# Kernel tuning notes

Measured on AMD Instinct MI355X. Metric: run time of the kernel, lower is better.

## Reference

```python
import jax, jax.numpy as jnp
import numpy as np

DIM = 1024
HEADS = 16
B, N = 4, 1024

def setup_inputs() -> dict:
    key = jax.random.key(0)
    k1, k2, k3 = jax.random.split(key, 3)
    x = jax.random.normal(k1, (B, N, DIM), dtype=jnp.float32)
    # xavier-uniform-ish init scale
    Wqkv = jax.random.normal(k2, (3 * DIM, DIM), dtype=jnp.float32) * (1.0 / np.sqrt(DIM))
    bqkv = jnp.zeros((3 * DIM,), dtype=jnp.float32)
    W1 = jax.random.normal(k3, (DIM, DIM), dtype=jnp.float32) * (1.0 / np.sqrt(DIM))
    b1 = jnp.zeros((DIM,), dtype=jnp.float32)
    return {"x": x, "Wqkv": Wqkv, "bqkv": bqkv, "W1": W1, "b1": b1}

def reference(x, Wqkv, bqkv, W1, b1):
    b, n, dim = x.shape
    h = HEADS
    d = dim // h
    scale = dim ** (-0.5)  # NOTE: module scales by full dim, not head dim
    qkv = x @ Wqkv.T + bqkv  # [b, n, 3*dim]
    qkv = qkv.reshape(b, n, 3, h, d)
    q = jnp.transpose(qkv[:, :, 0], (0, 2, 1, 3))  # [b, h, n, d]
    k = jnp.transpose(qkv[:, :, 1], (0, 2, 1, 3))
    v = jnp.transpose(qkv[:, :, 2], (0, 2, 1, 3))
    dots = jnp.einsum('bhid,bhjd->bhij', q, k) * scale
    attn = jax.nn.softmax(dots, axis=-1)
    out = jnp.einsum('bhij,bhjd->bhid', attn, v)
    out = jnp.transpose(out, (0, 2, 1, 3)).reshape(b, n, dim)
    out = out @ W1.T + b1
    return out
```

## Files before the change

kernel.cpp:

```cpp
#include <hip/hip_runtime.h>
#include <cmath>

typedef __bf16 bf16;
typedef __bf16 bf16x8 __attribute__((ext_vector_type(8)));
typedef __bf16 bf16x4 __attribute__((ext_vector_type(4)));
typedef float f32x4 __attribute__((ext_vector_type(4)));

#define MFMA16(a, b, c) __builtin_amdgcn_mfma_f32_16x16x32_bf16(a, b, c, 0, 0, 0)

__device__ __forceinline__ void load_lds16(const void* g, void* l) {
    __builtin_amdgcn_global_load_lds(
        (const __attribute__((address_space(1))) void*)g,
        (__attribute__((address_space(3))) void*)l, 16, 0, 0);
}

__device__ __forceinline__ bf16x8 load8(const bf16* p) { return *(const bf16x8*)p; }
__device__ __forceinline__ bf16x8 load8(const float* p) {
    float4 f0 = *(const float4*)p;
    float4 f1 = *(const float4*)(p + 4);
    bf16x8 r;
    r[0] = (bf16)f0.x; r[1] = (bf16)f0.y; r[2] = (bf16)f0.z; r[3] = (bf16)f0.w;
    r[4] = (bf16)f1.x; r[5] = (bf16)f1.y; r[6] = (bf16)f1.z; r[7] = (bf16)f1.w;
    return r;
}

__global__ __launch_bounds__(256) void cvt3(
    const float* __restrict__ s0, bf16* __restrict__ d0, int n0,
    const float* __restrict__ s1, bf16* __restrict__ d1, int n1,
    const float* __restrict__ s2, bf16* __restrict__ d2, int n2)
{
    int i = blockIdx.x * 256 + threadIdx.x;
    const float* s; bf16* d; int base;
    if (i < n0)                { s = s0; d = d0; base = i; }
    else if (i < n0 + n1)      { s = s1; d = d1; base = i - n0; }
    else if (i < n0 + n1 + n2) { s = s2; d = d2; base = i - n0 - n1; }
    else return;
    *(bf16x8*)(d + (size_t)base * 8) = load8(s + (size_t)base * 8);
}

template <int EPI, typename TB, int BN>
__global__ __launch_bounds__(256) void gemm_bt(
    const bf16* __restrict__ A, const TB* __restrict__ Bm,
    const float* __restrict__ bias,
    bf16* __restrict__ qo, bf16* __restrict__ ko, bf16* __restrict__ vto,
    float* __restrict__ C, int M, int N, int K)
{
    constexpr int WN = BN / 2;
    constexpr int JN = WN / 16;
    constexpr int SLOTS = (128 + BN) * 8;

    __shared__ bf16 As[128 * 64];
    __shared__ bf16 Bs[BN * 64];

    const int tid = threadIdx.x;
    const int l   = tid & 63;
    const int w   = tid >> 6;
    const int wm  = w & 1, wn = w >> 1;
    const int l15 = l & 15;
    const int g   = l >> 4;
    const int swz = l15 & 7;
    const int m0  = blockIdx.y * 128;
    const int n0  = blockIdx.x * BN;

    f32x4 acc[4][JN] = {};

    for (int k0 = 0; k0 < K; k0 += 64) {
        __syncthreads();
        #pragma unroll
        for (int it = 0; it < SLOTS / 256; ++it) {
            int s = it * 256 + w * 64 + l;
            if (s < 1024) {
                int row = s >> 3, pc = s & 7;
                int lc  = pc ^ (row & 7);
                load_lds16(A + (size_t)(m0 + row) * K + k0 + lc * 8, &As[s * 8]);
            } else {
                int t = s - 1024;
                int row = t >> 3, pc = t & 7;
                int lc  = pc ^ (row & 7);
                if constexpr (sizeof(TB) == 2) {
                    load_lds16(Bm + (size_t)(n0 + row) * K + k0 + lc * 8, &Bs[t * 8]);
                } else {
                    *(bf16x8*)&Bs[t * 8] = load8(Bm + (size_t)(n0 + row) * K + k0 + lc * 8);
                }
            }
        }
        __syncthreads();
        #pragma unroll
        for (int kk = 0; kk < 64; kk += 32) {
            bf16x8 aF[4], bF[JN];
            #pragma unroll
            for (int i = 0; i < 4; ++i)
                aF[i] = *(const bf16x8*)&As[(wm * 64 + i * 16 + l15) * 64
                                            + ((((kk >> 3) + g) ^ swz) * 8)];
            #pragma unroll
            for (int j = 0; j < JN; ++j)
                bF[j] = *(const bf16x8*)&Bs[(wn * WN + j * 16 + l15) * 64
                                            + ((((kk >> 3) + g) ^ swz) * 8)];
            #pragma unroll
            for (int i = 0; i < 4; ++i)
                #pragma unroll
                for (int j = 0; j < JN; ++j)
                    acc[i][j] = MFMA16(aF[i], bF[j], acc[i][j]);
        }
    }

    #pragma unroll
    for (int j = 0; j < JN; ++j) {
        int gcol = n0 + wn * WN + j * 16 + l15;
        float bv = bias[gcol];
        if (EPI == 0) {
            int which = gcol >> 10;
            int h  = (gcol >> 6) & 15;
            int dd = gcol & 63;
            #pragma unroll
            for (int i = 0; i < 4; ++i) {
                #pragma unroll
                for (int r = 0; r < 4; ++r) {
                    int grow = m0 + wm * 64 + i * 16 + g * 4 + r;
                    int b    = grow >> 10;
                    int npos = grow & 1023;
                    float v  = acc[i][j][r] + bv;
                    size_t bh = (size_t)(b * 16 + h);
                    if (which == 0)
                        qo[(bh * 1024 + npos) * 64 + dd] = (bf16)v;
                    else if (which == 1)
                        ko[(bh * 1024 + npos) * 64 + dd] = (bf16)v;
                    else
                        vto[(bh * 64 + dd) * 1024 + npos] = (bf16)v;
                }
            }
        } else {
            #pragma unroll
            for (int i = 0; i < 4; ++i)
                #pragma unroll
                for (int r = 0; r < 4; ++r) {
                    int grow = m0 + wm * 64 + i * 16 + g * 4 + r;
                    C[(size_t)grow * N + gcol] = acc[i][j][r] + bv;
                }
        }
    }
}

__global__ __launch_bounds__(256) void attn_fused(
    const bf16* __restrict__ qb, const bf16* __restrict__ kb,
    const bf16* __restrict__ vtb, bf16* __restrict__ attn)
{
    __shared__ bf16 Ks[64 * 64];
    __shared__ bf16 Vts[64 * 64];
    __shared__ bf16 Ps[4][32][72];

    const int tid = threadIdx.x;
    const int l   = tid & 63;
    const int w   = tid >> 6;
    const int l15 = l & 15;
    const int g   = l >> 4;
    const int swz = l15 & 7;
    const int bid = blockIdx.x;
    const int bh  = bid & 63;
    const int qc  = bid >> 6;
    const int m0  = qc * 128 + w * 32;

    const bf16* q_bh  = qb  + (size_t)bh * 65536;
    const bf16* k_bh  = kb  + (size_t)bh * 65536;
    const bf16* vt_bh = vtb + (size_t)bh * 65536;

    bf16x8 qf[2][2];
    #pragma unroll
    for (int mi = 0; mi < 2; ++mi)
        #pragma unroll
        for (int kk = 0; kk < 2; ++kk)
            qf[mi][kk] = *(const bf16x8*)(q_bh
                + (size_t)(m0 + mi * 16 + l15) * 64 + kk * 32 + g * 8);

    f32x4 o[2][4] = {};
    float lsum[2] = {0.f, 0.f};
    const float C_EXP = 0.04508422f;

    for (int jt = 0; jt < 16; ++jt) {
        const int j0 = jt * 64;
        __syncthreads();
        #pragma unroll
        for (int it = 0; it < 2; ++it) {
            int s   = it * 256 + tid;
            int row = s >> 3, pc = s & 7;
            int lc  = pc ^ (row & 7);
            load_lds16(k_bh + (size_t)(j0 + row) * 64 + lc * 8, &Ks[s * 8]);
            load_lds16(vt_bh + (size_t)row * 1024 + j0 + lc * 8, &Vts[s * 8]);
        }
        __syncthreads();

        bf16x8 kf[2][4], vf[2][4];
        #pragma unroll
        for (int kk = 0; kk < 2; ++kk)
            #pragma unroll
            for (int js = 0; js < 4; ++js) {
                int off = (js * 16 + l15) * 64 + (((kk * 4 + g) ^ swz) * 8);
                kf[kk][js] = *(const bf16x8*)&Ks[off];
                vf[kk][js] = *(const bf16x8*)&Vts[off];
            }

        #pragma unroll
        for (int mi = 0; mi < 2; ++mi) {
            f32x4 s4[4] = {};
            #pragma unroll
            for (int kk = 0; kk < 2; ++kk)
                #pragma unroll
                for (int js = 0; js < 4; ++js)
                    s4[js] = MFMA16(kf[kk][js], qf[mi][kk], s4[js]);
            float ls = 0.f;
            #pragma unroll
            for (int js = 0; js < 4; ++js) {
                bf16x4 pk;
                #pragma unroll
                for (int r = 0; r < 4; ++r) {
                    pk[r] = (bf16)exp2f(s4[js][r] * C_EXP);
                    ls += (float)pk[r];
                }
                *(bf16x4*)&Ps[w][mi * 16 + l15][js * 16 + g * 4] = pk;
            }
            lsum[mi] += ls;
        }
        __syncthreads();

        #pragma unroll
        for (int kk = 0; kk < 2; ++kk) {
            bf16x8 pf[2];
            #pragma unroll
            for (int mi = 0; mi < 2; ++mi)
                pf[mi] = *(const bf16x8*)&Ps[w][mi * 16 + l15][kk * 32 + g * 8];
            #pragma unroll
            for (int mi = 0; mi < 2; ++mi)
                #pragma unroll
                for (int ns = 0; ns < 4; ++ns)
                    o[mi][ns] = MFMA16(pf[mi], vf[kk][ns], o[mi][ns]);
        }
    }

    #pragma unroll
    for (int mi = 0; mi < 2; ++mi) {
        float t = lsum[mi];
        t += __shfl_xor(t, 16);
        t += __shfl_xor(t, 32);
        #pragma unroll
        for (int r = 0; r < 4; ++r) {
            float inv = 1.0f / __shfl(t, g * 4 + r);
            int grow = m0 + mi * 16 + g * 4 + r;
            size_t obase = ((size_t)(bh >> 4) * 1024 + grow) * 1024 + (bh & 15) * 64;
            #pragma unroll
            for (int ns = 0; ns < 4; ++ns)
                attn[obase + ns * 16 + l15] = (bf16)(o[mi][ns][r] * inv);
        }
    }
}

extern "C" void kernel_launch(void* const* d_in, const int* in_sizes, int n_in,
                              void* d_out, int out_size, void* d_ws, size_t ws_size,
                              hipStream_t stream)
{
    const float* x    = (const float*)d_in[0];
    const float* Wqkv = (const float*)d_in[1];
    const float* bqkv = (const float*)d_in[2];
    const float* W1   = (const float*)d_in[3];
    const float* b1   = (const float*)d_in[4];
    float* out = (float*)d_out;

    const size_t SEG = (size_t)4 * 16 * 1024 * 64;
    bf16* xbf  = (bf16*)d_ws;
    bf16* qb   = xbf + SEG;
    bf16* kb   = qb + SEG;
    bf16* vtb  = kb + SEG;
    bf16* attnb = xbf;
    bf16* wqkvbf = vtb + SEG;
    bf16* w1bf   = wqkvbf + 3145728;

    const bool cw = ws_size >= (size_t)(5 * SEG) * sizeof(bf16);

    const int nx = 524288;
    const int nw = cw ? 393216 : 0;
    const int n1 = cw ? 131072 : 0;
    const int tot = nx + nw + n1;
    cvt3<<<dim3((tot + 255) / 256), 256, 0, stream>>>(
        x, xbf, nx, Wqkv, wqkvbf, nw, W1, w1bf, n1);

    if (cw)
        gemm_bt<0, bf16, 128><<<dim3(24, 32), 256, 0, stream>>>(
            xbf, wqkvbf, bqkv, qb, kb, vtb, nullptr, 4096, 3072, 1024);
    else
        gemm_bt<0, float, 128><<<dim3(24, 32), 256, 0, stream>>>(
            xbf, Wqkv, bqkv, qb, kb, vtb, nullptr, 4096, 3072, 1024);

    attn_fused<<<dim3(512), 256, 0, stream>>>(qb, kb, vtb, attnb);

    if (cw)
        gemm_bt<1, bf16, 64><<<dim3(16, 32), 256, 0, stream>>>(
            attnb, w1bf, b1, nullptr, nullptr, nullptr, out, 4096, 1024, 1024);
    else
        gemm_bt<1, float, 64><<<dim3(16, 32), 256, 0, stream>>>(
            attnb, W1, b1, nullptr, nullptr, nullptr, out, 4096, 1024, 1024);
}
```

Before: 174.3 us.

## Halve attention query tile per block, double blocks, and load 128-key tiles

```diff
diff --git a/kernel.cpp b/kernel.cpp
--- a/kernel.cpp
+++ b/kernel.cpp
@@ -141,13 +141,13 @@
     }
 }
 
-__global__ __launch_bounds__(256) void attn_fused(
+__global__ __launch_bounds__(256, 4) void attn_fused(
     const bf16* __restrict__ qb, const bf16* __restrict__ kb,
     const bf16* __restrict__ vtb, bf16* __restrict__ attn)
 {
-    __shared__ bf16 Ks[64 * 64];
-    __shared__ bf16 Vts[64 * 64];
-    __shared__ bf16 Ps[4][32][72];
+    __shared__ __align__(16) bf16 Ks[2 * 64 * 64];
+    __shared__ __align__(16) bf16 Vts[2 * 64 * 64];
+    __shared__ __align__(16) bf16 Ps[4 * 16 * 64];
 
     const int tid = threadIdx.x;
     const int l   = tid & 63;
@@ -158,55 +158,58 @@
     const int bid = blockIdx.x;
     const int bh  = bid & 63;
     const int qc  = bid >> 6;
-    const int m0  = qc * 128 + w * 32;
+    const int m0  = qc * 64 + w * 16;
 
     const bf16* q_bh  = qb  + (size_t)bh * 65536;
     const bf16* k_bh  = kb  + (size_t)bh * 65536;
     const bf16* vt_bh = vtb + (size_t)bh * 65536;
 
-    bf16x8 qf[2][2];
+    bf16x8 qf[2];
     #pragma unroll
-    for (int mi = 0; mi < 2; ++mi)
-        #pragma unroll
-        for (int kk = 0; kk < 2; ++kk)
-            qf[mi][kk] = *(const bf16x8*)(q_bh
-                + (size_t)(m0 + mi * 16 + l15) * 64 + kk * 32 + g * 8);
-
-    f32x4 o[2][4] = {};
-    float lsum[2] = {0.f, 0.f};
+    for (int kk = 0; kk < 2; ++kk)
+        qf[kk] = *(const bf16x8*)(q_bh + (size_t)(m0 + l15) * 64 + kk * 32 + g * 8);
+
+    f32x4 o[4] = {};
+    float lsum = 0.f;
     const float C_EXP = 0.04508422f;
 
-    for (int jt = 0; jt < 16; ++jt) {
-        const int j0 = jt * 64;
-        __syncthreads();
-        #pragma unroll
-        for (int it = 0; it < 2; ++it) {
-            int s   = it * 256 + tid;
-            int row = s >> 3, pc = s & 7;
-            int lc  = pc ^ (row & 7);
-            load_lds16(k_bh + (size_t)(j0 + row) * 64 + lc * 8, &Ks[s * 8]);
-            load_lds16(vt_bh + (size_t)row * 1024 + j0 + lc * 8, &Vts[s * 8]);
-        }
-        __syncthreads();
-
-        bf16x8 kf[2][4], vf[2][4];
-        #pragma unroll
-        for (int kk = 0; kk < 2; ++kk)
-            #pragma unroll
-            for (int js = 0; js < 4; ++js) {
-                int off = (js * 16 + l15) * 64 + (((kk * 4 + g) ^ swz) * 8);
-                kf[kk][js] = *(const bf16x8*)&Ks[off];
-                vf[kk][js] = *(const bf16x8*)&Vts[off];
-            }
-
-        #pragma unroll
-        for (int mi = 0; mi < 2; ++mi) {
+    for (int jt = 0; jt < 8; ++jt) {
+        const int j0 = jt * 128;
+        __syncthreads();
+        #pragma unroll
+        for (int h = 0; h < 2; ++h)
+            #pragma unroll
+            for (int it = 0; it < 2; ++it) {
+                int s   = it * 256 + tid;
+                int row = s >> 3;
+                int lc  = (s & 7) ^ (row & 7);
+                load_lds16(k_bh + (size_t)(j0 + h * 64 + row) * 64 + lc * 8,
+                           &Ks[h * 4096 + s * 8]);
+                load_lds16(vt_bh + (size_t)row * 1024 + j0 + h * 64 + lc * 8,
+                           &Vts[h * 4096 + s * 8]);
+            }
+        __syncthreads();
+
+        #pragma unroll
+        for (int h = 0; h < 2; ++h) {
+            bf16x8 kf[2][4], vf[2][4];
+            #pragma unroll
+            for (int kk = 0; kk < 2; ++kk)
+                #pragma unroll
+                for (int js = 0; js < 4; ++js) {
+                    int off = h * 4096 + (js * 16 + l15) * 64
+                            + (((kk * 4 + g) ^ swz) * 8);
+                    kf[kk][js] = *(const bf16x8*)&Ks[off];
+                    vf[kk][js] = *(const bf16x8*)&Vts[off];
+                }
+
             f32x4 s4[4] = {};
             #pragma unroll
             for (int kk = 0; kk < 2; ++kk)
                 #pragma unroll
                 for (int js = 0; js < 4; ++js)
-                    s4[js] = MFMA16(kf[kk][js], qf[mi][kk], s4[js]);
+                    s4[js] = MFMA16(kf[kk][js], qf[kk], s4[js]);
+
             float ls = 0.f;
             #pragma unroll
             for (int js = 0; js < 4; ++js) {
@@ -216,40 +219,34 @@
                     pk[r] = (bf16)exp2f(s4[js][r] * C_EXP);
                     ls += (float)pk[r];
                 }
-                *(bf16x4*)&Ps[w][mi * 16 + l15][js * 16 + g * 4] = pk;
-            }
-            lsum[mi] += ls;
-        }
-        __syncthreads();
-
-        #pragma unroll
-        for (int kk = 0; kk < 2; ++kk) {
-            bf16x8 pf[2];
-            #pragma unroll
-            for (int mi = 0; mi < 2; ++mi)
-                pf[mi] = *(const bf16x8*)&Ps[w][mi * 16 + l15][kk * 32 + g * 8];
-            #pragma unroll
-            for (int mi = 0; mi < 2; ++mi)
+                int cw = (js * 2 + (g >> 1)) ^ swz;
+                *(bf16x4*)&Ps[w * 1024 + l15 * 64 + cw * 8 + (g & 1) * 4] = pk;
+            }
+            lsum += ls;
+            __syncthreads();
+
+            #pragma unroll
+            for (int kk = 0; kk < 2; ++kk) {
+                bf16x8 pf = *(const bf16x8*)&Ps[w * 1024 + l15 * 64
+                                                + (((kk * 4 + g) ^ swz) * 8)];
                 #pragma unroll
                 for (int ns = 0; ns < 4; ++ns)
-                    o[mi][ns] = MFMA16(pf[mi], vf[kk][ns], o[mi][ns]);
-        }
-    }
-
+                    o[ns] = MFMA16(pf, vf[kk][ns], o[ns]);
+            }
+        }
+    }
+
+    float t = lsum;
+    t += __shfl_xor(t, 16);
+    t += __shfl_xor(t, 32);
     #pragma unroll
-    for (int mi = 0; mi < 2; ++mi) {
-        float t = lsum[mi];
-        t += __shfl_xor(t, 16);
-        t += __shfl_xor(t, 32);
-        #pragma unroll
-        for (int r = 0; r < 4; ++r) {
-            float inv = 1.0f / __shfl(t, g * 4 + r);
-            int grow = m0 + mi * 16 + g * 4 + r;
-            size_t obase = ((size_t)(bh >> 4) * 1024 + grow) * 1024 + (bh & 15) * 64;
-            #pragma unroll
-            for (int ns = 0; ns < 4; ++ns)
-                attn[obase + ns * 16 + l15] = (bf16)(o[mi][ns][r] * inv);
-        }
+    for (int r = 0; r < 4; ++r) {
+        float inv = 1.0f / __shfl(t, g * 4 + r);
+        int grow = m0 + g * 4 + r;
+        size_t obase = ((size_t)(bh >> 4) * 1024 + grow) * 1024 + (bh & 15) * 64;
+        #pragma unroll
+        for (int ns = 0; ns < 4; ++ns)
+            attn[obase + ns * 16 + l15] = (bf16)(o[ns][r] * inv);
     }
 }
 
@@ -289,7 +286,7 @@
         gemm_bt<0, float, 128><<<dim3(24, 32), 256, 0, stream>>>(
             xbf, Wqkv, bqkv, qb, kb, vtb, nullptr, 4096, 3072, 1024);
 
-    attn_fused<<<dim3(512), 256, 0, stream>>>(qb, kb, vtb, attnb);
+    attn_fused<<<dim3(1024), 256, 0, stream>>>(qb, kb, vtb, attnb);
 
     if (cw)
         gemm_bt<1, bf16, 64><<<dim3(16, 32), 256, 0, stream>>>(
```

New measurement: 175.5 us. About the same (+0.7%).
